# Kernel optimization log

Hardware: AMD Instinct MI355X
Metric: run time of the kernel (lower is better)

The kernel has to match this reference:

```python
import jax, jax.numpy as jnp
import numpy as np

N_NODES = 100000
N_EDGES = 1600000
N_GRAPHS = 1000
IN_DIM, HID, OUT = 100, 128, 2


def setup_inputs() -> dict:
    key = jax.random.key(0)
    ks = jax.random.split(key, 9)
    x = jax.random.normal(ks[0], (N_NODES, IN_DIM), dtype=jnp.float32)
    edge_index = jax.random.randint(ks[1], (2, N_EDGES), 0, N_NODES, dtype=jnp.int64 if jax.config.jax_enable_x64 else jnp.int32)
    batch = jnp.sort(jax.random.randint(ks[2], (N_NODES,), 0, N_GRAPHS))
    W1 = jax.random.normal(ks[3], (IN_DIM, HID), dtype=jnp.float32) / np.sqrt(IN_DIM)
    b1 = jax.random.normal(ks[4], (HID,), dtype=jnp.float32) * 0.01
    W2 = jax.random.normal(ks[5], (HID, HID), dtype=jnp.float32) / np.sqrt(HID)
    b2 = jax.random.normal(ks[6], (HID,), dtype=jnp.float32) * 0.01
    Wfc = jax.random.normal(ks[7], (HID, OUT), dtype=jnp.float32) / np.sqrt(HID)
    bfc = jax.random.normal(ks[8], (OUT,), dtype=jnp.float32) * 0.01
    return {"x": x, "edge_index": edge_index, "batch": batch, "num_graphs": N_GRAPHS,
            "W1": W1, "b1": b1, "W2": W2, "b2": b2, "Wfc": Wfc, "bfc": bfc}


def reference(x, edge_index, batch, num_graphs, W1, b1, W2, b2, Wfc, bfc):
    n = x.shape[0]
    loop = jnp.arange(n, dtype=edge_index.dtype)
    # GCNConv default: add self loops, then symmetric normalization
    src = jnp.concatenate([edge_index[0], loop])  # [E+N]
    dst = jnp.concatenate([edge_index[1], loop])
    deg = jax.ops.segment_sum(jnp.ones_like(dst, dtype=x.dtype), dst, num_segments=n)  # in-degree incl self-loop
    dinv = jnp.where(deg > 0, jax.lax.rsqrt(deg), 0.0)
    norm = (dinv[src] * dinv[dst])[:, None]  # [E+N,1]

    def gcn_conv(h, W, b):
        h = h @ W                                # transform-first (small feat dim)
        msg = h[src] * norm                      # gather + scale  [E+N, F]
        agg = jax.ops.segment_sum(msg, dst, num_segments=n)  # scatter-add
        return agg + b

    h = jax.nn.relu(gcn_conv(x, W1, b1))
    h = jax.nn.relu(gcn_conv(h, W2, b2))

    # global_mean_pool over graphs
    sums = jax.ops.segment_sum(h, batch, num_segments=num_graphs)
    cnts = jax.ops.segment_sum(jnp.ones((n,), dtype=h.dtype), batch, num_segments=num_graphs)
    pooled = sums / jnp.maximum(cnts, 1.0)[:, None]
    # dropout is identity at inference
    return pooled @ Wfc + bfc
```

## Files before the change

kernel.cpp:

```cpp
#include <hip/hip_runtime.h>


#define GCN_GRAPHS 1000
#define CSR_CAP 64
#define BUCKET_CAP 4608
#define BIN_TILE 8192
#define POOL_CHUNKS 4

typedef short bf16x8 __attribute__((ext_vector_type(8)));
typedef float f32x4 __attribute__((ext_vector_type(4)));
typedef float f32x2 __attribute__((ext_vector_type(2)));

__device__ __forceinline__ unsigned short f2bf(float x) {
  unsigned u = __float_as_uint(x);
  return (unsigned short)((u + 0x7fff + ((u >> 16) & 1)) >> 16);
}
__device__ __forceinline__ f32x2 fp8x2_f32(unsigned short u) {
  return __builtin_amdgcn_cvt_pk_f32_fp8((int)(unsigned)u, false);
}
__device__ __forceinline__ unsigned char f32_fp8(float v) {
  return (unsigned char)(__builtin_amdgcn_cvt_pk_fp8_f32(v, v, 0, false) & 0xff);
}

__global__ __launch_bounds__(256) void setup_kernel(
    const float* __restrict__ W1, const float* __restrict__ W2,
    unsigned short* __restrict__ Wf1, unsigned short* __restrict__ Wf2,
    int* __restrict__ gcursor, int nbk, const int* __restrict__ batch,
    const float* __restrict__ bfc, float* __restrict__ out,
    float* __restrict__ invcnt, int* __restrict__ gstart,
    unsigned char* __restrict__ hs1, unsigned char* __restrict__ hs2,
    int N, int G) {
  int t = blockIdx.x * 256 + threadIdx.x;
  if (t < nbk) gcursor[t] = t * BUCKET_CAP;
  if (t < 32) {
    ((unsigned*)(hs1 + ((size_t)N << 7)))[t] = 0u;
    ((unsigned*)(hs2 + ((size_t)N << 7)))[t] = 0u;
  }
  if (t <= G) {
    int lo = 0, hi = N;
    while (lo < hi) { int mid = (lo + hi) >> 1; if (batch[mid] < t) lo = mid + 1; else hi = mid; }
    gstart[t] = lo;
    if (t < G) {
      int s = lo;
      hi = N;
      while (lo < hi) { int mid = (lo + hi) >> 1; if (batch[mid] < t + 1) lo = mid + 1; else hi = mid; }
      int cnt = lo - s;
      invcnt[t] = (cnt > 0) ? 1.f / (float)cnt : 0.f;
      out[2 * t + 0] = bfc[0];
      out[2 * t + 1] = bfc[1];
    }
  }
  for (int o = t; o < 16384; o += 4096) {
    int L = (o >> 3) & 63, j = o & 7;
    int tnq = o >> 9;
    int kq = tnq >> 3, tn = tnq & 7;
    int k = kq * 32 + (L >> 4) * 8 + j;
    int n = tn * 16 + (L & 15);
    Wf1[o] = (k < 100) ? f2bf(W1[k * 128 + n]) : (unsigned short)0;
    Wf2[o] = f2bf(W2[k * 128 + n]);
  }
}

__global__ __launch_bounds__(512) void bin_kernel(
    const int* __restrict__ src, const int* __restrict__ dst,
    int* __restrict__ gcursor, int* __restrict__ bucketbuf, int E, int nbk) {
  __shared__ int hist[512];
  __shared__ int off[512];
  __shared__ int gbase[512];
  __shared__ int lcur[512];
  __shared__ int wsum[8];
  __shared__ int stage[BIN_TILE];
  __shared__ int gofs[BIN_TILE];
  const int tid = threadIdx.x;
  const int lane = tid & 63, wv = tid >> 6;
  const int tile0 = blockIdx.x * BIN_TILE;
  int cnt = E - tile0;
  if (cnt > BIN_TILE) cnt = BIN_TILE;

  hist[tid] = 0;
  __syncthreads();
  for (int i = tid; i < cnt; i += 512) {
    int b = dst[tile0 + i] >> 8;
    atomicAdd(&hist[b], 1);
  }
  __syncthreads();
  int v = hist[tid];
  int inc = v;
#pragma unroll
  for (int s = 1; s < 64; s <<= 1) {
    int u = __shfl_up(inc, s);
    if (lane >= s) inc += u;
  }
  if (lane == 63) wsum[wv] = inc;
  __syncthreads();
  if (wv == 0 && lane < 8) {
    int p = wsum[lane];
#pragma unroll
    for (int s = 1; s < 8; s <<= 1) {
      int u = __shfl_up(p, s);
      if (lane >= s) p += u;
    }
    wsum[lane] = p;
  }
  __syncthreads();
  int excl = (wv ? wsum[wv - 1] : 0) + inc - v;
  off[tid] = excl;
  if (tid < nbk && v > 0)
    gbase[tid] = atomicAdd(&gcursor[tid], v);
  lcur[tid] = 0;
  __syncthreads();
  for (int i = tid; i < cnt; i += 512) {
    int d = dst[tile0 + i];
    int s = src[tile0 + i];
    int b = d >> 8;
    int r = atomicAdd(&lcur[b], 1);
    int pos = off[b] + r;
    stage[pos] = s | ((d & 255) << 17);
    int ga = gbase[b] + r;
    gofs[pos] = (ga < (b + 1) * BUCKET_CAP) ? ga : -1;
  }
  __syncthreads();
  for (int j = tid; j < cnt; j += 512) {
    int a = gofs[j];
    if (a >= 0) bucketbuf[a] = stage[j];
  }
}

__global__ __launch_bounds__(256) void build_kernel(
    const int* __restrict__ gcursor, const int* __restrict__ bucketbuf,
    int* __restrict__ csr, int* __restrict__ deg, int N) {
  __shared__ int lcnt[256];
  __shared__ int lcsr[256 * CSR_CAP];
  const int tid = threadIdx.x;
  const int b = blockIdx.x;
  const int base = b * BUCKET_CAP;
  int cnt = gcursor[b] - base;
  if (cnt > BUCKET_CAP) cnt = BUCKET_CAP;
  lcnt[tid] = 0;
  __syncthreads();
  for (int i = tid; i < cnt; i += 256) {
    int val = bucketbuf[base + i];
    int ld = val >> 17, s = val & 0x1FFFF;
    int r = atomicAdd(&lcnt[ld], 1);
    if (r < CSR_CAP) lcsr[ld * CSR_CAP + r] = s << 7;
  }
  __syncthreads();
  const int node0 = b << 8;
  int nb = N - node0;
  if (nb > 256) nb = 256;
  const uint4* ls = (const uint4*)lcsr;
  uint4* gd = (uint4*)(csr + (size_t)node0 * CSR_CAP);
  const int nq = nb * (CSR_CAP / 4);
  for (int j = tid; j < nq; j += 256) gd[j] = ls[j];
  if (tid < nb) deg[node0 + tid] = lcnt[tid];
}

__global__ __launch_bounds__(256) void gemm_mfma_f32(
    const float* __restrict__ A, const unsigned short* __restrict__ Wfrag,
    const int* __restrict__ deg, unsigned char* __restrict__ hs, int M) {
  __shared__ unsigned short As[128 * 128];
  __shared__ unsigned short Bs[128 * 128];
  const int tid = threadIdx.x;
  const int m0 = blockIdx.x * 128;

  {
    const uint4* sp = (const uint4*)Wfrag;
    uint4* dp = (uint4*)Bs;
#pragma unroll
    for (int u = 0; u < 8; ++u) dp[u * 256 + tid] = sp[u * 256 + tid];
  }
#pragma unroll
  for (int p = 0; p < 8; ++p) {
    int q = p * 256 + tid;
    int row = q >> 4;
    int c = q & 15;
    int rowg = m0 + row;
    int tm = row >> 4, mm = row & 15;
    int kq = c >> 2, quad = c & 3;
    unsigned short* ldst = As + (((tm * 4 + kq) * 64 + quad * 16 + mm) << 3);
    unsigned short tmp[8];
#pragma unroll
    for (int u = 0; u < 4; ++u) {
      int k = c * 8 + u * 2;
      float2 v = make_float2(0.f, 0.f);
      if (rowg < M && k < 100) v = *(const float2*)(A + (size_t)rowg * 100 + k);
      tmp[u * 2] = f2bf(v.x);
      tmp[u * 2 + 1] = f2bf(v.y);
    }
    *(uint4*)ldst = *(const uint4*)tmp;
  }
  __syncthreads();

  const int w = tid >> 6, lane = tid & 63;
  f32x4 acc[2][8];
#pragma unroll
  for (int r = 0; r < 2; ++r)
#pragma unroll
    for (int tn = 0; tn < 8; ++tn) acc[r][tn] = (f32x4){0.f, 0.f, 0.f, 0.f};

#pragma unroll
  for (int kq = 0; kq < 4; ++kq) {
    bf16x8 a0 = *(const bf16x8*)(As + ((((w * 2 + 0) * 4 + kq) * 64 + lane) << 3));
    bf16x8 a1 = *(const bf16x8*)(As + ((((w * 2 + 1) * 4 + kq) * 64 + lane) << 3));
#pragma unroll
    for (int tn = 0; tn < 8; ++tn) {
      bf16x8 b = *(const bf16x8*)(Bs + (((kq * 8 + tn) * 64 + lane) << 3));
      acc[0][tn] = __builtin_amdgcn_mfma_f32_16x16x32_bf16(a0, b, acc[0][tn], 0, 0, 0);
      acc[1][tn] = __builtin_amdgcn_mfma_f32_16x16x32_bf16(a1, b, acc[1][tn], 0, 0, 0);
    }
  }

  const int colb = lane & 15;
  const int rq = lane >> 4;
#pragma unroll
  for (int r = 0; r < 2; ++r) {
#pragma unroll
    for (int i = 0; i < 4; ++i) {
      int row = m0 + (w * 2 + r) * 16 + rq * 4 + i;
      if (row < M) {
        float dv = rsqrtf((float)deg[row] + 1.f);
        unsigned char* op = hs + (size_t)row * 128 + colb;
#pragma unroll
        for (int tn = 0; tn < 8; ++tn) op[tn * 16] = f32_fp8(acc[r][tn][i] * dv);
      }
    }
  }
}

__device__ __forceinline__ void gather_core4(
    const unsigned char* __restrict__ hs, const int* __restrict__ csr,
    int nodeQ, bool valid, int cnt, int mx, int Nshift, int qsel, int ql,
    float a[8]) {
  const unsigned qloff = (unsigned)(ql << 3);
  unsigned selfOff = (valid ? ((unsigned)nodeQ << 7) : (unsigned)Nshift) + qloff;
  uint2 su = *(const uint2*)(hs + selfOff);
  {
    f32x2 l0 = fp8x2_f32((unsigned short)su.x);
    f32x2 h0 = __builtin_amdgcn_cvt_pk_f32_fp8((int)su.x, true);
    f32x2 l1 = fp8x2_f32((unsigned short)su.y);
    f32x2 h1 = __builtin_amdgcn_cvt_pk_f32_fp8((int)su.y, true);
    a[0] = l0.x; a[1] = l0.y; a[2] = h0.x; a[3] = h0.y;
    a[4] = l1.x; a[5] = l1.y; a[6] = h1.x; a[7] = h1.y;
  }
  auto acc1 = [&](uint2 u) {
    f32x2 l0 = fp8x2_f32((unsigned short)u.x);
    f32x2 h0 = __builtin_amdgcn_cvt_pk_f32_fp8((int)u.x, true);
    f32x2 l1 = fp8x2_f32((unsigned short)u.y);
    f32x2 h1 = __builtin_amdgcn_cvt_pk_f32_fp8((int)u.y, true);
    a[0] += l0.x; a[1] += l0.y; a[2] += h0.x; a[3] += h0.y;
    a[4] += l1.x; a[5] += l1.y; a[6] += h1.x; a[7] += h1.y;
  };
  const int cbase = (valid ? nodeQ : 0) * CSR_CAP + ql;
#pragma unroll
  for (int j = 0; j < 4; ++j) {
    const int jb = j * 16;
    if (mx > jb) {
      int idx = (jb + ql < cnt) ? __builtin_nontemporal_load(csr + cbase + jb)
                                : Nshift;
      int lim = mx - jb;
      if (lim > 16) lim = 16;
      int s = 0;
      for (; s + 4 <= lim; s += 4) {
        int o0 = __builtin_amdgcn_ds_bpermute(qsel + ((s + 0) << 2), idx);
        int o1 = __builtin_amdgcn_ds_bpermute(qsel + ((s + 1) << 2), idx);
        int o2 = __builtin_amdgcn_ds_bpermute(qsel + ((s + 2) << 2), idx);
        int o3 = __builtin_amdgcn_ds_bpermute(qsel + ((s + 3) << 2), idx);
        uint2 u0 = *(const uint2*)(hs + ((unsigned)o0 + qloff));
        uint2 u1 = *(const uint2*)(hs + ((unsigned)o1 + qloff));
        uint2 u2 = *(const uint2*)(hs + ((unsigned)o2 + qloff));
        uint2 u3 = *(const uint2*)(hs + ((unsigned)o3 + qloff));
        acc1(u0); acc1(u1); acc1(u2); acc1(u3);
      }
      for (; s < lim; ++s) {
        int o0 = __builtin_amdgcn_ds_bpermute(qsel + (s << 2), idx);
        uint2 u0 = *(const uint2*)(hs + ((unsigned)o0 + qloff));
        acc1(u0);
      }
    }
  }
}

__global__ __launch_bounds__(512) void gemm2_fused(
    const unsigned char* __restrict__ hs1, const unsigned short* __restrict__ Wfrag,
    const int* __restrict__ deg, const int* __restrict__ csr,
    const float* __restrict__ b1, unsigned char* __restrict__ hs2, int M, int N) {
  __shared__ unsigned short As[128 * 128];
  __shared__ unsigned short Bs[128 * 128];
  const int tid = threadIdx.x;
  const int m0 = blockIdx.x * 128;
  const int wv = tid >> 6, lane = tid & 63;
  const int q = lane >> 4, ql = lane & 15;
  const int qsel = (lane & 48) << 2;
  const int Nshift = N << 7;

  {
    const uint4* sp = (const uint4*)Wfrag;
    uint4* dp = (uint4*)Bs;
#pragma unroll
    for (int u = 0; u < 4; ++u) dp[u * 512 + tid] = sp[u * 512 + tid];
  }

  const int fql = ql << 3;
  float4 bb0 = *(const float4*)(b1 + fql);
  float4 bb1 = *(const float4*)(b1 + fql + 4);
#pragma unroll
  for (int t = 0; t < 4; ++t) {
    const int row = t * 32 + wv * 4 + q;
    const int nodeQ = m0 + row;
    const bool valid = nodeQ < M;
    int dg = valid ? deg[nodeQ] : 0;
    int cnt = dg < CSR_CAP ? dg : CSR_CAP;
    int m = cnt;
    m = max(m, __shfl_xor(m, 16));
    m = max(m, __shfl_xor(m, 32));
    const int mx = __builtin_amdgcn_readfirstlane(m);

    float a[8];
    gather_core4(hs1, csr, nodeQ, valid, cnt, mx, Nshift, qsel, ql, a);

    float dv = rsqrtf((float)dg + 1.f);
    unsigned short h[8];
    if (valid) {
      h[0] = f2bf(fmaxf(fmaf(dv, a[0], bb0.x), 0.f));
      h[1] = f2bf(fmaxf(fmaf(dv, a[1], bb0.y), 0.f));
      h[2] = f2bf(fmaxf(fmaf(dv, a[2], bb0.z), 0.f));
      h[3] = f2bf(fmaxf(fmaf(dv, a[3], bb0.w), 0.f));
      h[4] = f2bf(fmaxf(fmaf(dv, a[4], bb1.x), 0.f));
      h[5] = f2bf(fmaxf(fmaf(dv, a[5], bb1.y), 0.f));
      h[6] = f2bf(fmaxf(fmaf(dv, a[6], bb1.z), 0.f));
      h[7] = f2bf(fmaxf(fmaf(dv, a[7], bb1.w), 0.f));
    } else {
#pragma unroll
      for (int k = 0; k < 8; ++k) h[k] = 0;
    }
    unsigned short* ldst =
        As + ((((row >> 4) * 4 + (ql >> 2)) * 64 + (ql & 3) * 16 + (row & 15)) << 3);
    *(uint4*)ldst = *(const uint4*)h;
  }
  __syncthreads();

  f32x4 acc[8];
#pragma unroll
  for (int tn = 0; tn < 8; ++tn) acc[tn] = (f32x4){0.f, 0.f, 0.f, 0.f};
#pragma unroll
  for (int kq = 0; kq < 4; ++kq) {
    bf16x8 av = *(const bf16x8*)(As + (((wv * 4 + kq) * 64 + lane) << 3));
#pragma unroll
    for (int tn = 0; tn < 8; ++tn) {
      bf16x8 b = *(const bf16x8*)(Bs + (((kq * 8 + tn) * 64 + lane) << 3));
      acc[tn] = __builtin_amdgcn_mfma_f32_16x16x32_bf16(av, b, acc[tn], 0, 0, 0);
    }
  }

  const int colb = lane & 15;
  const int rq = lane >> 4;
#pragma unroll
  for (int i = 0; i < 4; ++i) {
    int row = m0 + wv * 16 + rq * 4 + i;
    if (row < M) {
      float dv = rsqrtf((float)deg[row] + 1.f);
      unsigned char* op = hs2 + (size_t)row * 128 + colb;
#pragma unroll
      for (int tn = 0; tn < 8; ++tn) op[tn * 16] = f32_fp8(acc[tn][i] * dv);
    }
  }
}

__global__ __launch_bounds__(256) void gatherpool_kernel(
    const unsigned char* __restrict__ hs, const int* __restrict__ deg,
    const int* __restrict__ csr, const float* __restrict__ b2,
    const int* __restrict__ gstart, const float* __restrict__ Wfc,
    const float* __restrict__ invcnt, float* __restrict__ out, int N) {
  __shared__ float part[4][128];
  const int g = blockIdx.x / POOL_CHUNKS;
  const int chunk = blockIdx.x % POOL_CHUNKS;
  const int tid = threadIdx.x, lane = tid & 63, wv = tid >> 6;
  const int q = lane >> 4, ql = lane & 15;
  const int qsel = (lane & 48) << 2;
  const int s = gstart[g], e = gstart[g + 1];
  const int Nshift = N << 7;
  const int f = ql << 3;
  float4 bb0 = *(const float4*)(b2 + f);
  float4 bb1 = *(const float4*)(b2 + f + 4);
  float p[8];
#pragma unroll
  for (int k = 0; k < 8; ++k) p[k] = 0.f;

  for (int d = s + (chunk * 4 + wv) * 4; d < e; d += 4 * 4 * POOL_CHUNKS) {
    const int nodeQ = d + q;
    const bool valid = nodeQ < e;
    int dg = valid ? deg[nodeQ] : 0;
    int cnt = dg < CSR_CAP ? dg : CSR_CAP;
    int m = cnt;
    m = max(m, __shfl_xor(m, 16));
    m = max(m, __shfl_xor(m, 32));
    const int mx = __builtin_amdgcn_readfirstlane(m);

    float a[8];
    gather_core4(hs, csr, nodeQ, valid, cnt, mx, Nshift, qsel, ql, a);

    float dv = rsqrtf((float)dg + 1.f);
    if (valid) {
      p[0] += fmaxf(fmaf(dv, a[0], bb0.x), 0.f);
      p[1] += fmaxf(fmaf(dv, a[1], bb0.y), 0.f);
      p[2] += fmaxf(fmaf(dv, a[2], bb0.z), 0.f);
      p[3] += fmaxf(fmaf(dv, a[3], bb0.w), 0.f);
      p[4] += fmaxf(fmaf(dv, a[4], bb1.x), 0.f);
      p[5] += fmaxf(fmaf(dv, a[5], bb1.y), 0.f);
      p[6] += fmaxf(fmaf(dv, a[6], bb1.z), 0.f);
      p[7] += fmaxf(fmaf(dv, a[7], bb1.w), 0.f);
    }
  }
#pragma unroll
  for (int k = 0; k < 8; ++k) {
    p[k] += __shfl_xor(p[k], 16);
    p[k] += __shfl_xor(p[k], 32);
  }
  if (q == 0) {
#pragma unroll
    for (int k = 0; k < 8; ++k) part[wv][f + k] = p[k];
  }
  __syncthreads();
  if (wv == 0) {
    int f2 = lane * 2;
    float ax = part[0][f2] + part[1][f2] + part[2][f2] + part[3][f2];
    float ay = part[0][f2 + 1] + part[1][f2 + 1] + part[2][f2 + 1] + part[3][f2 + 1];
    float ic = invcnt[g];
    float mx = ax * ic, my = ay * ic;
    float s0 = mx * Wfc[f2 * 2 + 0] + my * Wfc[f2 * 2 + 2];
    float s1 = mx * Wfc[f2 * 2 + 1] + my * Wfc[f2 * 2 + 3];
#pragma unroll
    for (int off = 32; off > 0; off >>= 1) {
      s0 += __shfl_down(s0, off);
      s1 += __shfl_down(s1, off);
    }
    if (lane == 0) {
      atomicAdd(&out[2 * g + 0], s0);
      atomicAdd(&out[2 * g + 1], s1);
    }
  }
}

extern "C" void kernel_launch(void* const* d_in, const int* in_sizes, int n_in,
                              void* d_out, int out_size, void* d_ws, size_t ws_size,
                              hipStream_t stream) {
  const float* x   = (const float*)d_in[0];
  const int*   ei  = (const int*)d_in[1];
  const int*   bat = (const int*)d_in[2];
  const float* W1  = (const float*)d_in[4];
  const float* b1  = (const float*)d_in[5];
  const float* W2  = (const float*)d_in[6];
  const float* b2  = (const float*)d_in[7];
  const float* Wfc = (const float*)d_in[8];
  const float* bfc = (const float*)d_in[9];

  const int N = in_sizes[2];
  const int E = in_sizes[1] / 2;
  const int G = GCN_GRAPHS;
  const int* src = ei;
  const int* dst = ei + E;
  const int nbk = (N + 255) >> 8;

  char* w = (char*)d_ws;
  auto carve = [&](size_t bytes) {
    void* p = (void*)w;
    w += (bytes + 15) & ~(size_t)15;
    return p;
  };
  int* deg       = (int*)carve((size_t)N * 4);
  int* gcursor   = (int*)carve((size_t)nbk * 4);
  float* invcnt  = (float*)carve((size_t)G * 4);
  int* gstart    = (int*)carve((size_t)(G + 1) * 4);
  unsigned short* Wf1 = (unsigned short*)carve(16384 * 2);
  unsigned short* Wf2 = (unsigned short*)carve(16384 * 2);
  int* bucketbuf = (int*)carve((size_t)nbk * BUCKET_CAP * 4);
  int* csr       = (int*)carve((size_t)N * CSR_CAP * 4);
  unsigned char* bufA = (unsigned char*)carve((size_t)(N + 1) * 128);
  unsigned char* bufC = (unsigned char*)carve((size_t)(N + 1) * 128);
  (void)ws_size; (void)n_in; (void)out_size;

  setup_kernel<<<16, 256, 0, stream>>>(W1, W2, Wf1, Wf2, gcursor, nbk, bat, bfc,
                                       (float*)d_out, invcnt, gstart, bufA, bufC, N, G);
  bin_kernel<<<(E + BIN_TILE - 1) / BIN_TILE, 512, 0, stream>>>(src, dst, gcursor,
                                                                bucketbuf, E, nbk);
  build_kernel<<<nbk, 256, 0, stream>>>(gcursor, bucketbuf, csr, deg, N);

  const int gemmBlocks = (N + 127) / 128;

  gemm_mfma_f32<<<gemmBlocks, 256, 0, stream>>>(x, Wf1, deg, bufA, N);

  gemm2_fused<<<gemmBlocks, 512, 0, stream>>>(bufA, Wf2, deg, csr, b1, bufC, N, N);

  gatherpool_kernel<<<G * POOL_CHUNKS, 256, 0, stream>>>(bufC, deg, csr, b2, gstart,
                                                         Wfc, invcnt, (float*)d_out, N);
}
```

Measured before the change: 269.4 us.

## Replace two-pass bucketed CSR build with direct atomic scatter fused into setup

```diff
diff --git a/kernel.cpp b/kernel.cpp
--- a/kernel.cpp
+++ b/kernel.cpp
@@ -3,8 +3,6 @@
 
 #define GCN_GRAPHS 1000
 #define CSR_CAP 64
-#define BUCKET_CAP 4608
-#define BIN_TILE 8192
 #define POOL_CHUNKS 4
 
 typedef short bf16x8 __attribute__((ext_vector_type(8)));
@@ -22,137 +20,54 @@
   return (unsigned char)(__builtin_amdgcn_cvt_pk_fp8_f32(v, v, 0, false) & 0xff);
 }
 
-__global__ __launch_bounds__(256) void setup_kernel(
+__global__ __launch_bounds__(256) void scatter_setup_kernel(
+    const int* __restrict__ src, const int* __restrict__ dst,
+    int* __restrict__ deg, int* __restrict__ csr, int E, int scatBlocks,
     const float* __restrict__ W1, const float* __restrict__ W2,
     unsigned short* __restrict__ Wf1, unsigned short* __restrict__ Wf2,
-    int* __restrict__ gcursor, int nbk, const int* __restrict__ batch,
-    const float* __restrict__ bfc, float* __restrict__ out,
-    float* __restrict__ invcnt, int* __restrict__ gstart,
-    unsigned char* __restrict__ hs1, unsigned char* __restrict__ hs2,
-    int N, int G) {
-  int t = blockIdx.x * 256 + threadIdx.x;
-  if (t < nbk) gcursor[t] = t * BUCKET_CAP;
-  if (t < 32) {
-    ((unsigned*)(hs1 + ((size_t)N << 7)))[t] = 0u;
-    ((unsigned*)(hs2 + ((size_t)N << 7)))[t] = 0u;
-  }
-  if (t <= G) {
-    int lo = 0, hi = N;
-    while (lo < hi) { int mid = (lo + hi) >> 1; if (batch[mid] < t) lo = mid + 1; else hi = mid; }
-    gstart[t] = lo;
-    if (t < G) {
-      int s = lo;
-      hi = N;
-      while (lo < hi) { int mid = (lo + hi) >> 1; if (batch[mid] < t + 1) lo = mid + 1; else hi = mid; }
-      int cnt = lo - s;
-      invcnt[t] = (cnt > 0) ? 1.f / (float)cnt : 0.f;
-      out[2 * t + 0] = bfc[0];
-      out[2 * t + 1] = bfc[1];
-    }
-  }
-  for (int o = t; o < 16384; o += 4096) {
-    int L = (o >> 3) & 63, j = o & 7;
-    int tnq = o >> 9;
-    int kq = tnq >> 3, tn = tnq & 7;
-    int k = kq * 32 + (L >> 4) * 8 + j;
-    int n = tn * 16 + (L & 15);
-    Wf1[o] = (k < 100) ? f2bf(W1[k * 128 + n]) : (unsigned short)0;
-    Wf2[o] = f2bf(W2[k * 128 + n]);
-  }
-}
-
-__global__ __launch_bounds__(512) void bin_kernel(
-    const int* __restrict__ src, const int* __restrict__ dst,
-    int* __restrict__ gcursor, int* __restrict__ bucketbuf, int E, int nbk) {
-  __shared__ int hist[512];
-  __shared__ int off[512];
-  __shared__ int gbase[512];
-  __shared__ int lcur[512];
-  __shared__ int wsum[8];
-  __shared__ int stage[BIN_TILE];
-  __shared__ int gofs[BIN_TILE];
+    const int* __restrict__ batch, const float* __restrict__ bfc,
+    float* __restrict__ out, float* __restrict__ invcnt,
+    int* __restrict__ gstart, unsigned char* __restrict__ hs1,
+    unsigned char* __restrict__ hs2, int N, int G) {
   const int tid = threadIdx.x;
-  const int lane = tid & 63, wv = tid >> 6;
-  const int tile0 = blockIdx.x * BIN_TILE;
-  int cnt = E - tile0;
-  if (cnt > BIN_TILE) cnt = BIN_TILE;
-
-  hist[tid] = 0;
-  __syncthreads();
-  for (int i = tid; i < cnt; i += 512) {
-    int b = dst[tile0 + i] >> 8;
-    atomicAdd(&hist[b], 1);
-  }
-  __syncthreads();
-  int v = hist[tid];
-  int inc = v;
-#pragma unroll
-  for (int s = 1; s < 64; s <<= 1) {
-    int u = __shfl_up(inc, s);
-    if (lane >= s) inc += u;
-  }
-  if (lane == 63) wsum[wv] = inc;
-  __syncthreads();
-  if (wv == 0 && lane < 8) {
-    int p = wsum[lane];
-#pragma unroll
-    for (int s = 1; s < 8; s <<= 1) {
-      int u = __shfl_up(p, s);
-      if (lane >= s) p += u;
-    }
-    wsum[lane] = p;
-  }
-  __syncthreads();
-  int excl = (wv ? wsum[wv - 1] : 0) + inc - v;
-  off[tid] = excl;
-  if (tid < nbk && v > 0)
-    gbase[tid] = atomicAdd(&gcursor[tid], v);
-  lcur[tid] = 0;
-  __syncthreads();
-  for (int i = tid; i < cnt; i += 512) {
-    int d = dst[tile0 + i];
-    int s = src[tile0 + i];
-    int b = d >> 8;
-    int r = atomicAdd(&lcur[b], 1);
-    int pos = off[b] + r;
-    stage[pos] = s | ((d & 255) << 17);
-    int ga = gbase[b] + r;
-    gofs[pos] = (ga < (b + 1) * BUCKET_CAP) ? ga : -1;
-  }
-  __syncthreads();
-  for (int j = tid; j < cnt; j += 512) {
-    int a = gofs[j];
-    if (a >= 0) bucketbuf[a] = stage[j];
-  }
-}
-
-__global__ __launch_bounds__(256) void build_kernel(
-    const int* __restrict__ gcursor, const int* __restrict__ bucketbuf,
-    int* __restrict__ csr, int* __restrict__ deg, int N) {
-  __shared__ int lcnt[256];
-  __shared__ int lcsr[256 * CSR_CAP];
-  const int tid = threadIdx.x;
-  const int b = blockIdx.x;
-  const int base = b * BUCKET_CAP;
-  int cnt = gcursor[b] - base;
-  if (cnt > BUCKET_CAP) cnt = BUCKET_CAP;
-  lcnt[tid] = 0;
-  __syncthreads();
-  for (int i = tid; i < cnt; i += 256) {
-    int val = bucketbuf[base + i];
-    int ld = val >> 17, s = val & 0x1FFFF;
-    int r = atomicAdd(&lcnt[ld], 1);
-    if (r < CSR_CAP) lcsr[ld * CSR_CAP + r] = s << 7;
-  }
-  __syncthreads();
-  const int node0 = b << 8;
-  int nb = N - node0;
-  if (nb > 256) nb = 256;
-  const uint4* ls = (const uint4*)lcsr;
-  uint4* gd = (uint4*)(csr + (size_t)node0 * CSR_CAP);
-  const int nq = nb * (CSR_CAP / 4);
-  for (int j = tid; j < nq; j += 256) gd[j] = ls[j];
-  if (tid < nb) deg[node0 + tid] = lcnt[tid];
+  if ((int)blockIdx.x >= scatBlocks) {
+    int t = ((int)blockIdx.x - scatBlocks) * 256 + tid;
+    if (t < 32) {
+      ((unsigned*)(hs1 + ((size_t)N << 7)))[t] = 0u;
+      ((unsigned*)(hs2 + ((size_t)N << 7)))[t] = 0u;
+    }
+    if (t <= G) {
+      int lo = 0, hi = N;
+      while (lo < hi) { int mid = (lo + hi) >> 1; if (batch[mid] < t) lo = mid + 1; else hi = mid; }
+      gstart[t] = lo;
+      if (t < G) {
+        int s = lo;
+        hi = N;
+        while (lo < hi) { int mid = (lo + hi) >> 1; if (batch[mid] < t + 1) lo = mid + 1; else hi = mid; }
+        int cnt = lo - s;
+        invcnt[t] = (cnt > 0) ? 1.f / (float)cnt : 0.f;
+        out[2 * t + 0] = bfc[0];
+        out[2 * t + 1] = bfc[1];
+      }
+    }
+    for (int o = t; o < 16384; o += 2048) {
+      int L = (o >> 3) & 63, j = o & 7;
+      int tnq = o >> 9;
+      int kq = tnq >> 3, tn = tnq & 7;
+      int k = kq * 32 + (L >> 4) * 8 + j;
+      int n = tn * 16 + (L & 15);
+      Wf1[o] = (k < 100) ? f2bf(W1[k * 128 + n]) : (unsigned short)0;
+      Wf2[o] = f2bf(W2[k * 128 + n]);
+    }
+    return;
+  }
+  const int stride = scatBlocks * 256;
+  for (int i = (int)blockIdx.x * 256 + tid; i < E; i += stride) {
+    int d = dst[i];
+    int s = src[i];
+    int pos = atomicAdd(&deg[d], 1);
+    if (pos < CSR_CAP) csr[d * CSR_CAP + pos] = s << 7;
+  }
 }
 
 __global__ __launch_bounds__(256) void gemm_mfma_f32(
@@ -459,7 +374,6 @@
   const int G = GCN_GRAPHS;
   const int* src = ei;
   const int* dst = ei + E;
-  const int nbk = (N + 255) >> 8;
 
   char* w = (char*)d_ws;
   auto carve = [&](size_t bytes) {
@@ -468,22 +382,21 @@
     return p;
   };
   int* deg       = (int*)carve((size_t)N * 4);
-  int* gcursor   = (int*)carve((size_t)nbk * 4);
   float* invcnt  = (float*)carve((size_t)G * 4);
   int* gstart    = (int*)carve((size_t)(G + 1) * 4);
   unsigned short* Wf1 = (unsigned short*)carve(16384 * 2);
   unsigned short* Wf2 = (unsigned short*)carve(16384 * 2);
-  int* bucketbuf = (int*)carve((size_t)nbk * BUCKET_CAP * 4);
   int* csr       = (int*)carve((size_t)N * CSR_CAP * 4);
   unsigned char* bufA = (unsigned char*)carve((size_t)(N + 1) * 128);
   unsigned char* bufC = (unsigned char*)carve((size_t)(N + 1) * 128);
   (void)ws_size; (void)n_in; (void)out_size;
 
-  setup_kernel<<<16, 256, 0, stream>>>(W1, W2, Wf1, Wf2, gcursor, nbk, bat, bfc,
-                                       (float*)d_out, invcnt, gstart, bufA, bufC, N, G);
-  bin_kernel<<<(E + BIN_TILE - 1) / BIN_TILE, 512, 0, stream>>>(src, dst, gcursor,
-                                                                bucketbuf, E, nbk);
-  build_kernel<<<nbk, 256, 0, stream>>>(gcursor, bucketbuf, csr, deg, N);
+  hipMemsetAsync(deg, 0, (size_t)N * 4, stream);
+
+  const int scatBlocks = 2048;
+  scatter_setup_kernel<<<scatBlocks + 8, 256, 0, stream>>>(
+      src, dst, deg, csr, E, scatBlocks,
+      W1, W2, Wf1, Wf2, bat, bfc, (float*)d_out, invcnt, gstart, bufA, bufC, N, G);
 
   const int gemmBlocks = (N + 127) / 128;
 
```

Result: slower. 366.4 us (+36.0%).

## Fuse setup into bin kernel and halve bin tile size

Applied to the files above, without the earlier changes.

```diff
diff --git a/kernel.cpp b/kernel.cpp
--- a/kernel.cpp
+++ b/kernel.cpp
@@ -4,7 +4,7 @@
 #define GCN_GRAPHS 1000
 #define CSR_CAP 64
 #define BUCKET_CAP 4608
-#define BIN_TILE 8192
+#define BIN_TILE 4096
 #define POOL_CHUNKS 4
 
 typedef short bf16x8 __attribute__((ext_vector_type(8)));
@@ -22,48 +22,48 @@
   return (unsigned char)(__builtin_amdgcn_cvt_pk_fp8_f32(v, v, 0, false) & 0xff);
 }
 
-__global__ __launch_bounds__(256) void setup_kernel(
+__global__ __launch_bounds__(512) void bin_setup_kernel(
+    const int* __restrict__ src, const int* __restrict__ dst,
+    int* __restrict__ gcursor, int* __restrict__ bucketbuf, int E, int nbk,
+    int binBlocks,
     const float* __restrict__ W1, const float* __restrict__ W2,
     unsigned short* __restrict__ Wf1, unsigned short* __restrict__ Wf2,
-    int* __restrict__ gcursor, int nbk, const int* __restrict__ batch,
-    const float* __restrict__ bfc, float* __restrict__ out,
-    float* __restrict__ invcnt, int* __restrict__ gstart,
-    unsigned char* __restrict__ hs1, unsigned char* __restrict__ hs2,
-    int N, int G) {
-  int t = blockIdx.x * 256 + threadIdx.x;
-  if (t < nbk) gcursor[t] = t * BUCKET_CAP;
-  if (t < 32) {
-    ((unsigned*)(hs1 + ((size_t)N << 7)))[t] = 0u;
-    ((unsigned*)(hs2 + ((size_t)N << 7)))[t] = 0u;
-  }
-  if (t <= G) {
-    int lo = 0, hi = N;
-    while (lo < hi) { int mid = (lo + hi) >> 1; if (batch[mid] < t) lo = mid + 1; else hi = mid; }
-    gstart[t] = lo;
-    if (t < G) {
-      int s = lo;
-      hi = N;
-      while (lo < hi) { int mid = (lo + hi) >> 1; if (batch[mid] < t + 1) lo = mid + 1; else hi = mid; }
-      int cnt = lo - s;
-      invcnt[t] = (cnt > 0) ? 1.f / (float)cnt : 0.f;
-      out[2 * t + 0] = bfc[0];
-      out[2 * t + 1] = bfc[1];
-    }
-  }
-  for (int o = t; o < 16384; o += 4096) {
-    int L = (o >> 3) & 63, j = o & 7;
-    int tnq = o >> 9;
-    int kq = tnq >> 3, tn = tnq & 7;
-    int k = kq * 32 + (L >> 4) * 8 + j;
-    int n = tn * 16 + (L & 15);
-    Wf1[o] = (k < 100) ? f2bf(W1[k * 128 + n]) : (unsigned short)0;
-    Wf2[o] = f2bf(W2[k * 128 + n]);
-  }
-}
-
-__global__ __launch_bounds__(512) void bin_kernel(
-    const int* __restrict__ src, const int* __restrict__ dst,
-    int* __restrict__ gcursor, int* __restrict__ bucketbuf, int E, int nbk) {
+    const int* __restrict__ batch, const float* __restrict__ bfc,
+    float* __restrict__ out, float* __restrict__ invcnt,
+    int* __restrict__ gstart, unsigned char* __restrict__ hs1,
+    unsigned char* __restrict__ hs2, int N, int G) {
+  const int tid = threadIdx.x;
+  if ((int)blockIdx.x >= binBlocks) {
+    int t = ((int)blockIdx.x - binBlocks) * 512 + tid;
+    if (t < 32) {
+      ((unsigned*)(hs1 + ((size_t)N << 7)))[t] = 0u;
+      ((unsigned*)(hs2 + ((size_t)N << 7)))[t] = 0u;
+    }
+    if (t <= G) {
+      int lo = 0, hi = N;
+      while (lo < hi) { int mid = (lo + hi) >> 1; if (batch[mid] < t) lo = mid + 1; else hi = mid; }
+      gstart[t] = lo;
+      if (t < G) {
+        int s = lo;
+        hi = N;
+        while (lo < hi) { int mid = (lo + hi) >> 1; if (batch[mid] < t + 1) lo = mid + 1; else hi = mid; }
+        int cnt = lo - s;
+        invcnt[t] = (cnt > 0) ? 1.f / (float)cnt : 0.f;
+        out[2 * t + 0] = bfc[0];
+        out[2 * t + 1] = bfc[1];
+      }
+    }
+    for (int o = t; o < 16384; o += 4096) {
+      int L = (o >> 3) & 63, j = o & 7;
+      int tnq = o >> 9;
+      int kq = tnq >> 3, tn = tnq & 7;
+      int k = kq * 32 + (L >> 4) * 8 + j;
+      int n = tn * 16 + (L & 15);
+      Wf1[o] = (k < 100) ? f2bf(W1[k * 128 + n]) : (unsigned short)0;
+      Wf2[o] = f2bf(W2[k * 128 + n]);
+    }
+    return;
+  }
   __shared__ int hist[512];
   __shared__ int off[512];
   __shared__ int gbase[512];
@@ -71,7 +71,6 @@
   __shared__ int wsum[8];
   __shared__ int stage[BIN_TILE];
   __shared__ int gofs[BIN_TILE];
-  const int tid = threadIdx.x;
   const int lane = tid & 63, wv = tid >> 6;
   const int tile0 = blockIdx.x * BIN_TILE;
   int cnt = E - tile0;
@@ -106,7 +105,7 @@
   int excl = (wv ? wsum[wv - 1] : 0) + inc - v;
   off[tid] = excl;
   if (tid < nbk && v > 0)
-    gbase[tid] = atomicAdd(&gcursor[tid], v);
+    gbase[tid] = tid * BUCKET_CAP + atomicAdd(&gcursor[tid], v);
   lcur[tid] = 0;
   __syncthreads();
   for (int i = tid; i < cnt; i += 512) {
@@ -134,7 +133,7 @@
   const int tid = threadIdx.x;
   const int b = blockIdx.x;
   const int base = b * BUCKET_CAP;
-  int cnt = gcursor[b] - base;
+  int cnt = gcursor[b];
   if (cnt > BUCKET_CAP) cnt = BUCKET_CAP;
   lcnt[tid] = 0;
   __syncthreads();
@@ -479,10 +478,13 @@
   unsigned char* bufC = (unsigned char*)carve((size_t)(N + 1) * 128);
   (void)ws_size; (void)n_in; (void)out_size;
 
-  setup_kernel<<<16, 256, 0, stream>>>(W1, W2, Wf1, Wf2, gcursor, nbk, bat, bfc,
-                                       (float*)d_out, invcnt, gstart, bufA, bufC, N, G);
-  bin_kernel<<<(E + BIN_TILE - 1) / BIN_TILE, 512, 0, stream>>>(src, dst, gcursor,
-                                                                bucketbuf, E, nbk);
+  hipMemsetAsync(gcursor, 0, (size_t)nbk * 4, stream);
+
+  const int binBlocks = (E + BIN_TILE - 1) / BIN_TILE;
+  bin_setup_kernel<<<binBlocks + 8, 512, 0, stream>>>(
+      src, dst, gcursor, bucketbuf, E, nbk, binBlocks,
+      W1, W2, Wf1, Wf2, bat, bfc, (float*)d_out, invcnt, gstart, bufA, bufC, N, G);
+
   build_kernel<<<nbk, 256, 0, stream>>>(gcursor, bucketbuf, csr, deg, N);
 
   const int gemmBlocks = (N + 127) / 128;
```

After: 268.1 us. Within noise of the previous version (-0.5%).
